# Performance work log

Measured on AMD Instinct MI355X. Metric: run time of the kernel, lower is better.

The kernel has to match this reference:

```python
import jax, jax.numpy as jnp
import numpy as np

B, H, L, N, DT_EMB, EXPAND = 8, 256, 8192, 16, 512, 2


def _tln(x, m, s):
    # TransposedLN: std/mean over channel dim (-2), population std
    mean = x.mean(axis=-2, keepdims=True)
    std = jnp.sqrt(((x - mean) ** 2).mean(axis=-2, keepdims=True))
    return s / std * (x - mean + m)


def _s4(u, log_dt, A_re, A_im, C_re, C_im, D, out_w, out_b):
    # Bidirectional diagonal S4 (S4D-style ZOH kernel) with FFT convolution.
    h, l = u.shape[-2], u.shape[-1]
    A = A_re + 1j * A_im                                   # (H, N)
    dtA = A * jnp.exp(log_dt)[:, None]                     # (H, N)
    C = (C_re + 1j * C_im) * (jnp.exp(dtA) - 1.0) / A      # (2, H, N)
    van = jnp.exp(dtA[:, :, None] * jnp.arange(l))         # (H, N, L) Vandermonde
    K = 2.0 * jnp.einsum('chn,hnl->chl', C, van).real      # (2, H, L)
    # bidirectional: forward kernel + time-flipped backward kernel, length 2L
    k = jnp.pad(K[0], ((0, 0), (0, l))) + jnp.pad(K[1][:, ::-1], ((0, 0), (l, 0)))
    y = jnp.fft.irfft(jnp.fft.rfft(u, n=2 * l) * jnp.fft.rfft(k, n=2 * l), n=2 * l)[..., :l]
    y = jax.nn.gelu(y + u * D[:, None])
    # transposed output linear (1x1 conv) H -> 2H, then GLU over channels
    z = jnp.einsum('oh,bhl->bol', out_w, y) + out_b[None, :, None]
    return z[:, :h] * jax.nn.sigmoid(z[:, h:])


def setup_inputs() -> dict:
    key = jax.random.key(0)
    ks = jax.random.split(key, 12)
    d_inner = EXPAND * H
    log_dt = jax.random.uniform(ks[0], (H,)) * (np.log(0.1) - np.log(0.001)) + np.log(0.001)
    return {
        'x': jax.random.normal(ks[1], (B, H, L), dtype=jnp.float32),
        'diffusion_step_embed': jax.random.normal(ks[2], (B, DT_EMB), dtype=jnp.float32),
        'fc_t_w': jax.random.normal(ks[3], (H, DT_EMB), dtype=jnp.float32) * 0.02,
        'fc_t_b': jnp.zeros((H,), dtype=jnp.float32),
        'log_dt': log_dt.astype(jnp.float32),
        'A_re': -0.5 * jnp.ones((H, N), dtype=jnp.float32),
        'A_im': jnp.broadcast_to(np.pi * jnp.arange(N, dtype=jnp.float32), (H, N)),
        'C_re': jax.random.normal(ks[4], (2, H, N), dtype=jnp.float32) * (0.5 ** 0.5),
        'C_im': jax.random.normal(ks[5], (2, H, N), dtype=jnp.float32) * (0.5 ** 0.5),
        'D': jax.random.normal(ks[6], (H,), dtype=jnp.float32),
        'out_w': jax.random.normal(ks[7], (2 * H, H), dtype=jnp.float32) * 0.02,
        'out_b': jnp.zeros((2 * H,), dtype=jnp.float32),
        'n1_m': jnp.zeros((), dtype=jnp.float32),
        'n1_s': jnp.ones((), dtype=jnp.float32),
        'n2_m': jnp.zeros((), dtype=jnp.float32),
        'n2_s': jnp.ones((), dtype=jnp.float32),
        'ff_w1': jax.random.normal(ks[8], (d_inner, H), dtype=jnp.float32) * 0.05,
        'ff_b1': jnp.zeros((d_inner,), dtype=jnp.float32),
        'ff_w2': jax.random.normal(ks[9], (H, d_inner), dtype=jnp.float32) * 0.05,
        'ff_b2': jnp.zeros((H,), dtype=jnp.float32),
    }


def reference(x, diffusion_step_embed, fc_t_w, fc_t_b, log_dt, A_re, A_im, C_re, C_im, D,
              out_w, out_b, n1_m, n1_s, n2_m, n2_s, ff_w1, ff_b1, ff_w2, ff_b2):
    y = _tln(x, n1_m, n1_s)
    part_t = diffusion_step_embed @ fc_t_w.T + fc_t_b      # (B, H)
    y = y + part_t[:, :, None]
    y = _s4(y, log_dt, A_re, A_im, C_re, C_im, D, out_w, out_b)
    y = x + y                                              # residual 1
    res = y
    y = _tln(y, n2_m, n2_s)
    h = jax.nn.gelu(jnp.einsum('oh,bhl->bol', ff_w1, y) + ff_b1[None, :, None])
    y = jnp.einsum('ho,bol->bhl', ff_w2, h) + ff_b2[None, :, None]
    return res + y
```

## Files before the change

kernel.cpp:

```cpp
#include <hip/hip_runtime.h>
#include <hip/hip_bf16.h>
#include <math.h>

typedef unsigned short u16;
typedef float fx4 __attribute__((ext_vector_type(4)));
typedef __bf16 bx8 __attribute__((ext_vector_type(8)));

constexpr int BB  = 8;
constexpr int HH  = 256;
constexpr int LL  = 8192;
constexpr int NN  = 16;
constexpr int DTE = 512;
constexpr int SC  = 64;
constexpr int CHN = 128;
constexpr int HN  = HH * NN;

constexpr size_t BHL = (size_t)BB * HH * LL;

constexpr int OFF_WR  = 0;
constexpr int OFF_WI  = HN;
constexpr int OFF_WSR = 2 * HN;
constexpr int OFF_WSI = 3 * HN;
constexpr int OFF_C0R = 4 * HN;
constexpr int OFF_C0I = 5 * HN;
constexpr int OFF_C1R = 6 * HN;
constexpr int OFF_C1I = 7 * HN;
constexpr int OFF_PT  = 8 * HN;

constexpr int PM_V2H = 0;
constexpr int PM_V2L = 4096;
constexpr int PM_TH  = 8192;
constexpr int PM_TL  = 12288;
constexpr int PM_CWH = 16384;
constexpr int PM_CWL = 20480;
constexpr int PM_STRIDE = 24576;

__device__ __forceinline__ float gelu_tanh(float x) {
    float x3 = x * x * x;
    float y = 1.5957691216057308f * x + 0.07135481627767453f * x3;
    return x / (1.0f + __expf(-y));
}
__device__ __forceinline__ float sigmoid_(float x) {
    return 1.0f / (1.0f + __expf(-x));
}
__device__ __forceinline__ __hip_bfloat16 f2b(float x) { return __float2bfloat16(x); }
__device__ __forceinline__ float b2f(__hip_bfloat16 x) { return __bfloat162float(x); }
__device__ __forceinline__ u16 f2us(float x) {
    __hip_bfloat16 b = __float2bfloat16(x);
    return *reinterpret_cast<u16*>(&b);
}
__device__ __forceinline__ float lo2f(unsigned v) { return __uint_as_float(v << 16); }
__device__ __forceinline__ float hi2f(unsigned v) { return __uint_as_float(v & 0xffff0000u); }
__device__ __forceinline__ unsigned pack2(float a, float b) {
    return (unsigned)f2us(a) | ((unsigned)f2us(b) << 16);
}

__global__ void setup_s4_params(const float* __restrict__ log_dt,
                                const float* __restrict__ A_re,
                                const float* __restrict__ A_im,
                                const float* __restrict__ C_re,
                                const float* __restrict__ C_im,
                                float* __restrict__ P) {
    int idx = blockIdx.x * blockDim.x + threadIdx.x;
    if (idx >= HN) return;
    int h = idx >> 4;
    double dt = exp((double)log_dt[h]);
    double Ar = (double)A_re[idx], Ai = (double)A_im[idx];
    double dr = Ar * dt, di = Ai * dt;
    double e1 = exp(dr);
    double wr = e1 * cos(di), wi = e1 * sin(di);
    double eS = exp(dr * SC);
    double wSr = eS * cos(di * SC), wSi = eS * sin(di * SC);
    double d2 = Ar * Ar + Ai * Ai;
    double nr = wr - 1.0, ni = wi;
    double rr = (nr * Ar + ni * Ai) / d2;
    double ri = (ni * Ar - nr * Ai) / d2;
    double c0r = (double)C_re[idx],        c0i = (double)C_im[idx];
    double c1r = (double)C_re[HN + idx],   c1i = (double)C_im[HN + idx];
    P[OFF_WR  + idx] = (float)wr;
    P[OFF_WI  + idx] = (float)wi;
    P[OFF_WSR + idx] = (float)wSr;
    P[OFF_WSI + idx] = (float)wSi;
    P[OFF_C0R + idx] = (float)(2.0 * (c0r * rr - c0i * ri));
    P[OFF_C0I + idx] = (float)(2.0 * (c0r * ri + c0i * rr));
    P[OFF_C1R + idx] = (float)(2.0 * (c1r * rr - c1i * ri));
    P[OFF_C1I + idx] = (float)(2.0 * (c1r * ri + c1i * rr));
}

__global__ void setup_scan_mats(const float* __restrict__ P,
                                const float* __restrict__ Dp,
                                u16* __restrict__ PM) {
    const int h = blockIdx.x;
    const int t = threadIdx.x;
    __shared__ float Wr[65][17], Wi[65][17];
    __shared__ float KF[64], KB[64];
    __shared__ float c0r[16], c0i[16], c1r[16], c1i[16];
    if (t < 16) {
        c0r[t] = P[OFF_C0R + h * NN + t]; c0i[t] = P[OFF_C0I + h * NN + t];
        c1r[t] = P[OFF_C1R + h * NN + t]; c1i[t] = P[OFF_C1I + h * NN + t];
        double wr = (double)P[OFF_WR + h * NN + t], wi = (double)P[OFF_WI + h * NN + t];
        double pr = 1.0, pi = 0.0;
        for (int tau = 0; tau <= 64; ++tau) {
            Wr[tau][t] = (float)pr; Wi[tau][t] = (float)pi;
            double nr = pr * wr - pi * wi, ni = pr * wi + pi * wr;
            pr = nr; pi = ni;
        }
    }
    __syncthreads();
    {
        float kf = 0.f, kb = 0.f;
        #pragma unroll
        for (int n = 0; n < 16; ++n) {
            kf = fmaf(c0r[n], Wr[t][n], fmaf(-c0i[n], Wi[t][n], kf));
            kb = fmaf(c1r[n], Wr[t][n], fmaf(-c1i[n], Wi[t][n], kb));
        }
        KF[t] = kf; KB[t] = kb;
    }
    __syncthreads();
    u16* base = PM + (size_t)h * PM_STRIDE;
    {
        int n = (t & 31) >> 1, reim = t & 1;
        bool fwd = t < 32;
        for (int j = 0; j < 64; ++j) {
            int e = fwd ? (63 - j) : j;
            float v = reim ? Wi[e][n] : Wr[e][n];
            __hip_bfloat16 hb = f2b(v);
            base[PM_V2H + t * 64 + j] = *(u16*)&hb;
            base[PM_V2L + t * 64 + j] = f2us(v - b2f(hb));
        }
    }
    {
        float Dh = Dp[h];
        for (int j = 0; j < 64; ++j) {
            float v = (j < t) ? KF[t - j] : ((j == t) ? (KF[0] + Dh) : KB[j - t - 1]);
            __hip_bfloat16 hb = f2b(v);
            base[PM_TH + t * 64 + j] = *(u16*)&hb;
            base[PM_TL + t * 64 + j] = f2us(v - b2f(hb));
        }
    }
    {
        #pragma unroll
        for (int n = 0; n < 16; ++n) {
            float Rw = Wr[t + 1][n], Iw = Wi[t + 1][n];
            float af = fmaf(c0r[n], Rw, -c0i[n] * Iw);
            float bf = -fmaf(c0r[n], Iw, c0i[n] * Rw);
            float Rb = Wr[63 - t][n], Ib = Wi[63 - t][n];
            float ab = fmaf(c1r[n], Rb, -c1i[n] * Ib);
            float bb = -fmaf(c1r[n], Ib, c1i[n] * Rb);
            float vals[4] = {af, bf, ab, bb};
            int cols[4] = {2 * n, 2 * n + 1, 32 + 2 * n, 32 + 2 * n + 1};
            #pragma unroll
            for (int q = 0; q < 4; ++q) {
                __hip_bfloat16 hb = f2b(vals[q]);
                base[PM_CWH + t * 64 + cols[q]] = *(u16*)&hb;
                base[PM_CWL + t * 64 + cols[q]] = f2us(vals[q] - b2f(hb));
            }
        }
    }
}

__global__ void part_t_kernel(const float* __restrict__ emb,
                              const float* __restrict__ w,
                              const float* __restrict__ bias,
                              float* __restrict__ P) {
    int idx = blockIdx.x * blockDim.x + threadIdx.x;
    if (idx >= BB * HH) return;
    int b = idx / HH, h = idx % HH;
    float s = bias[h];
    const float* er = emb + (size_t)b * DTE;
    const float* wr = w + (size_t)h * DTE;
    for (int e = 0; e < DTE; ++e) s = fmaf(er[e], wr[e], s);
    P[OFF_PT + idx] = s;
}

__global__ void convert_w_kernel(const float* __restrict__ src, u16* __restrict__ dst, int n) {
    int i = blockIdx.x * 256 + threadIdx.x;
    if (i < n) dst[i] = f2us(src[i]);
}

__global__ void convert_w_split(const float* __restrict__ src,
                                u16* __restrict__ hi, u16* __restrict__ lo, int n) {
    int i = blockIdx.x * 256 + threadIdx.x;
    if (i < n) {
        float v = src[i];
        __hip_bfloat16 hb = f2b(v);
        hi[i] = *reinterpret_cast<u16*>(&hb);
        lo[i] = f2us(v - b2f(hb));
    }
}

__global__ void tln_kernel(const float* __restrict__ in, float* __restrict__ out,
                           const float* __restrict__ mptr, const float* __restrict__ sptr,
                           const float* __restrict__ part_t) {
    int b = blockIdx.y;
    int l0 = blockIdx.x * 64;
    int t = threadIdx.x;
    int q = t >> 6, li = t & 63;
    const float* base = in + (size_t)b * HH * LL + l0 + li;
    float sum = 0.f, sq = 0.f;
    for (int i = 0; i < 64; ++i) {
        float v = base[(size_t)(q * 64 + i) * LL];
        sum += v; sq = fmaf(v, v, sq);
    }
    __shared__ float rs[4][64], rq[4][64], meanS[64], scaleS[64];
    rs[q][li] = sum; rq[q][li] = sq;
    __syncthreads();
    if (q == 0) {
        float s  = rs[0][li] + rs[1][li] + rs[2][li] + rs[3][li];
        float s2 = rq[0][li] + rq[1][li] + rq[2][li] + rq[3][li];
        float mean = s * (1.f / 256.f);
        float var  = fmaxf(s2 * (1.f / 256.f) - mean * mean, 0.f);
        meanS[li]  = mean;
        scaleS[li] = sptr[0] / sqrtf(var);
    }
    __syncthreads();
    float mean = meanS[li], scale = scaleS[li], m = mptr[0];
    float* ob = out + (size_t)b * HH * LL + l0 + li;
    for (int i = 0; i < 64; ++i) {
        int h = q * 64 + i;
        float v = base[(size_t)h * LL];
        float y = scale * (v - mean + m) + part_t[b * HH + h];
        ob[(size_t)h * LL] = y;
    }
}

__global__ void tln2t_kernel(const float* __restrict__ in, u16* __restrict__ outT,
                             const float* __restrict__ mptr, const float* __restrict__ sptr) {
    int b = blockIdx.y;
    int l0 = blockIdx.x * 64;
    int t = threadIdx.x;
    int q = t >> 6, li = t & 63;
    const float* base = in + (size_t)b * HH * LL + l0 + li;
    float sum = 0.f, sq = 0.f;
    for (int i = 0; i < 64; ++i) {
        float v = base[(size_t)(q * 64 + i) * LL];
        sum += v; sq = fmaf(v, v, sq);
    }
    __shared__ float rs[4][64], rq[4][64], meanS[64], scaleS[64];
    __shared__ u16 TT[64 * 262];
    rs[q][li] = sum; rq[q][li] = sq;
    __syncthreads();
    if (q == 0) {
        float s  = rs[0][li] + rs[1][li] + rs[2][li] + rs[3][li];
        float s2 = rq[0][li] + rq[1][li] + rq[2][li] + rq[3][li];
        float mean = s * (1.f / 256.f);
        float var  = fmaxf(s2 * (1.f / 256.f) - mean * mean, 0.f);
        meanS[li]  = mean;
        scaleS[li] = sptr[0] / sqrtf(var);
    }
    __syncthreads();
    float mean = meanS[li], scale = scaleS[li], m = mptr[0];
    for (int i = 0; i < 64; ++i) {
        int h = q * 64 + i;
        float v = base[(size_t)h * LL];
        TT[li * 262 + h] = f2us(scale * (v - mean + m));
    }
    __syncthreads();
    #pragma unroll
    for (int i = 0; i < 32; ++i) {
        int idx = t + i * 256;
        int c = idx & 127, l = idx >> 7;
        unsigned int v = *(const unsigned int*)&TT[l * 262 + 2 * c];
        *(unsigned int*)&outT[((size_t)b * LL + l0 + l) * 256 + 2 * c] = v;
    }
}

constexpr int UPAD = 136;
constexpr int SPAD = 72;

__global__ __launch_bounds__(256, 3) void scan_mfma(
    const float* __restrict__ uIn, const float* __restrict__ P,
    const u16* __restrict__ PM, float* __restrict__ ys)
{
    __shared__ __align__(16) u16 U[128 * UPAD];
    __shared__ __align__(16) u16 SES[128 * SPAD];

    const int bh  = blockIdx.x;
    const int h   = bh & (HH - 1);
    const int tid = threadIdx.x;
    const int lane = tid & 63;
    const int wq   = tid >> 6;
    const u16* pm = PM + (size_t)h * PM_STRIDE;
    const float* urow = uIn + (size_t)bh * LL;
    float* yrow = ys + (size_t)bh * LL;

    {
        const float4* u4 = (const float4*)urow;
        #pragma unroll
        for (int i = 0; i < 8; ++i) {
            int e4 = tid + i * 256;
            float4 v = u4[e4];
            int g = e4 << 2, c = g >> 6, j = g & 63;
            u16 hi4[4], lo4[4];
            #pragma unroll
            for (int q = 0; q < 4; ++q) {
                float f = (&v.x)[q];
                __hip_bfloat16 hb = f2b(f);
                hi4[q] = *(u16*)&hb;
                lo4[q] = f2us(f - b2f(hb));
            }
            *(ushort4*)&U[c * UPAD + j]      = *(ushort4*)hi4;
            *(ushort4*)&U[c * UPAD + 64 + j] = *(ushort4*)lo4;
        }
    }
    __syncthreads();

    const int cb    = wq * 32 + (lane & 15);
    const int kfrag = ((lane >> 4) & 3) * 8;
    const int arow_lo = lane & 15;

    bx8 ubh[2][2], ubl[2][2];
    #pragma unroll
    for (int nt = 0; nt < 2; ++nt) {
        int c = cb + nt * 16;
        #pragma unroll
        for (int ks = 0; ks < 2; ++ks) {
            ubh[nt][ks] = *(const bx8*)&U[c * UPAD + ks * 32 + kfrag];
            ubl[nt][ks] = *(const bx8*)&U[c * UPAD + 64 + ks * 32 + kfrag];
        }
    }

    {
        fx4 acc[4][2];
        #pragma unroll
        for (int mt = 0; mt < 4; ++mt)
            #pragma unroll
            for (int nt = 0; nt < 2; ++nt) { fx4 z = {0.f,0.f,0.f,0.f}; acc[mt][nt] = z; }
        #pragma unroll
        for (int mt = 0; mt < 4; ++mt) {
            #pragma unroll
            for (int ks = 0; ks < 2; ++ks) {
                int ao = (mt * 16 + arow_lo) * 64 + ks * 32 + kfrag;
                bx8 vh = *(const bx8*)&pm[PM_V2H + ao];
                bx8 vl = *(const bx8*)&pm[PM_V2L + ao];
                #pragma unroll
                for (int nt = 0; nt < 2; ++nt) {
                    acc[mt][nt] = __builtin_amdgcn_mfma_f32_16x16x32_bf16(vh, ubh[nt][ks], acc[mt][nt], 0, 0, 0);
                    acc[mt][nt] = __builtin_amdgcn_mfma_f32_16x16x32_bf16(vh, ubl[nt][ks], acc[mt][nt], 0, 0, 0);
                    acc[mt][nt] = __builtin_amdgcn_mfma_f32_16x16x32_bf16(vl, ubh[nt][ks], acc[mt][nt], 0, 0, 0);
                }
            }
        }
        #pragma unroll
        for (int mt = 0; mt < 4; ++mt)
            #pragma unroll
            for (int nt = 0; nt < 2; ++nt) {
                int c = cb + nt * 16;
                int row = mt * 16 + (lane >> 4) * 4;
                #pragma unroll
                for (int r = 0; r < 4; ++r)
                    SES[c * SPAD + row + r] = f2us(acc[mt][nt][r]);
            }
    }
    __syncthreads();

    if (tid < 32) {
        const int d3 = tid >> 4, n = tid & 15;
        float wSr = P[OFF_WSR + h * NN + n], wSi = P[OFF_WSI + h * NN + n];
        const int kk = d3 * 32 + 2 * n;
        float cr = 0.f, ci = 0.f;
        if (d3 == 0) {
            for (int q = 0; q < CHN; ++q) {
                unsigned* p = (unsigned*)&SES[q * SPAD + kk];
                unsigned pv = *p;
                float fr = lo2f(pv), fi = hi2f(pv);
                *p = pack2(cr, ci);
                float nr2 = fmaf(wSr, cr, fmaf(-wSi, ci, fr));
                float ni2 = fmaf(wSr, ci, fmaf(wSi, cr, fi));
                cr = nr2; ci = ni2;
            }
        } else {
            for (int q = CHN - 1; q >= 0; --q) {
                unsigned* p = (unsigned*)&SES[q * SPAD + kk];
                unsigned pv = *p;
                float fr = lo2f(pv), fi = hi2f(pv);
                *p = pack2(cr, ci);
                float nr2 = fmaf(wSr, cr, fmaf(-wSi, ci, fr));
                float ni2 = fmaf(wSr, ci, fmaf(wSi, cr, fi));
                cr = nr2; ci = ni2;
            }
        }
    }
    __syncthreads();

    {
        bx8 sb[2][2];
        #pragma unroll
        for (int nt = 0; nt < 2; ++nt) {
            int c = cb + nt * 16;
            #pragma unroll
            for (int ks = 0; ks < 2; ++ks)
                sb[nt][ks] = *(const bx8*)&SES[c * SPAD + ks * 32 + kfrag];
        }
        fx4 acc[4][2];
        #pragma unroll
        for (int mt = 0; mt < 4; ++mt)
            #pragma unroll
            for (int nt = 0; nt < 2; ++nt) { fx4 z = {0.f,0.f,0.f,0.f}; acc[mt][nt] = z; }
        #pragma unroll
        for (int mt = 0; mt < 4; ++mt) {
            #pragma unroll
            for (int ks = 0; ks < 2; ++ks) {
                int ao = (mt * 16 + arow_lo) * 64 + ks * 32 + kfrag;
                bx8 th = *(const bx8*)&pm[PM_TH + ao];
                bx8 tl = *(const bx8*)&pm[PM_TL + ao];
                bx8 ch = *(const bx8*)&pm[PM_CWH + ao];
                bx8 cl = *(const bx8*)&pm[PM_CWL + ao];
                #pragma unroll
                for (int nt = 0; nt < 2; ++nt) {
                    acc[mt][nt] = __builtin_amdgcn_mfma_f32_16x16x32_bf16(th, ubh[nt][ks], acc[mt][nt], 0, 0, 0);
                    acc[mt][nt] = __builtin_amdgcn_mfma_f32_16x16x32_bf16(th, ubl[nt][ks], acc[mt][nt], 0, 0, 0);
                    acc[mt][nt] = __builtin_amdgcn_mfma_f32_16x16x32_bf16(tl, ubh[nt][ks], acc[mt][nt], 0, 0, 0);
                    acc[mt][nt] = __builtin_amdgcn_mfma_f32_16x16x32_bf16(ch, sb[nt][ks], acc[mt][nt], 0, 0, 0);
                    acc[mt][nt] = __builtin_amdgcn_mfma_f32_16x16x32_bf16(cl, sb[nt][ks], acc[mt][nt], 0, 0, 0);
                }
            }
        }
        #pragma unroll
        for (int mt = 0; mt < 4; ++mt)
            #pragma unroll
            for (int nt = 0; nt < 2; ++nt) {
                int c = cb + nt * 16;
                float4 ov;
                #pragma unroll
                for (int r = 0; r < 4; ++r)
                    (&ov.x)[r] = gelu_tanh(acc[mt][nt][r]);
                *(float4*)&yrow[c * 64 + mt * 16 + (lane >> 4) * 4] = ov;
            }
    }
}

__global__ __launch_bounds__(256, 2) void gemm_glu_mfma(
    const u16* __restrict__ Whi, const u16* __restrict__ Wlo,
    const float* __restrict__ Y, const float* __restrict__ bias,
    const float* __restrict__ xres, float* __restrict__ out)
{
    __shared__ __align__(16) char smem[65536];
    u16* Ah = (u16*)smem;
    u16* Al = Ah + 8192;
    u16* Bh = Al + 8192;
    u16* Bl = Bh + 8192;

    const int tid  = threadIdx.x;
    const int lane = tid & 63;
    const int wv   = tid >> 6;
    const int wrh  = wv & 1;
    const int wch  = wv >> 1;
    const int bz   = blockIdx.z;
    const int l0   = blockIdx.x * 128;
    const int c0   = blockIdx.y * 64;

    fx4 acc[4][4];
    #pragma unroll
    for (int i = 0; i < 4; ++i)
        #pragma unroll
        for (int j = 0; j < 4; ++j) {
            fx4 z = {0.f, 0.f, 0.f, 0.f};
            acc[i][j] = z;
        }

    const int am  = tid & 127;
    const int akh = tid >> 7;
    const int aorow = (am < 64) ? (c0 + am) : (c0 + 256 + (am - 64));
    const int amt = am >> 4, amm = am & 15;

    const int bli = (tid & 63) + ((tid >> 6) & 1) * 64;
    const int bkh = tid >> 7;
    const int bnt = bli >> 4, bcol = bli & 15;

    const float* Yb = Y + (size_t)bz * HH * LL + l0;

    for (int k0 = 0; k0 < 256; k0 += 64) {
        #pragma unroll
        for (int oct = 0; oct < 4; ++oct) {
            int k = k0 + akh * 32 + oct * 8;
            int4 vh = *(const int4*)&Whi[(size_t)aorow * 256 + k];
            int4 vl = *(const int4*)&Wlo[(size_t)aorow * 256 + k];
            int base = ((akh * 8 + amt) * 64 + amm + (oct << 4)) * 8;
            *(int4*)&Ah[base] = vh;
            *(int4*)&Al[base] = vl;
        }
        #pragma unroll
        for (int oct = 0; oct < 4; ++oct) {
            int kb = k0 + bkh * 32 + oct * 8;
            float v[8];
            #pragma unroll
            for (int j = 0; j < 8; ++j)
                v[j] = Yb[(size_t)(kb + j) * LL + bli];
            u16 h8[8], l8[8];
            #pragma unroll
            for (int j = 0; j < 8; ++j) {
                __hip_bfloat16 hb = f2b(v[j]);
                h8[j] = *reinterpret_cast<u16*>(&hb);
                l8[j] = f2us(v[j] - b2f(hb));
            }
            int base = ((bkh * 8 + bnt) * 64 + bcol + (oct << 4)) * 8;
            *(int4*)&Bh[base] = *(const int4*)h8;
            *(int4*)&Bl[base] = *(const int4*)l8;
        }
        __syncthreads();
        #pragma unroll
        for (int ks = 0; ks < 2; ++ks) {
            bx8 bh[4], bl[4];
            #pragma unroll
            for (int nt = 0; nt < 4; ++nt) {
                int base = ((ks * 8 + wch * 4 + nt) * 64 + lane) * 8;
                bh[nt] = *(const bx8*)&Bh[base];
                bl[nt] = *(const bx8*)&Bl[base];
            }
            #pragma unroll
            for (int mt = 0; mt < 4; ++mt) {
                int base = ((ks * 8 + wrh * 4 + mt) * 64 + lane) * 8;
                bx8 ah = *(const bx8*)&Ah[base];
                bx8 al = *(const bx8*)&Al[base];
                #pragma unroll
                for (int nt = 0; nt < 4; ++nt) {
                    acc[mt][nt] = __builtin_amdgcn_mfma_f32_16x16x32_bf16(ah, bh[nt], acc[mt][nt], 0, 0, 0);
                    acc[mt][nt] = __builtin_amdgcn_mfma_f32_16x16x32_bf16(ah, bl[nt], acc[mt][nt], 0, 0, 0);
                    acc[mt][nt] = __builtin_amdgcn_mfma_f32_16x16x32_bf16(al, bh[nt], acc[mt][nt], 0, 0, 0);
                }
            }
        }
        __syncthreads();
    }

    float* zbuf = (float*)smem;
    if (wrh == 1) {
        #pragma unroll
        for (int mt = 0; mt < 4; ++mt) {
            int mloc = mt * 16 + (lane >> 4) * 4;
            float b1v[4];
            #pragma unroll
            for (int r = 0; r < 4; ++r) b1v[r] = bias[c0 + 256 + mloc + r];
            #pragma unroll
            for (int nt = 0; nt < 4; ++nt) {
                int nloc = nt * 16 + (lane & 15);
                #pragma unroll
                for (int r = 0; r < 4; ++r)
                    zbuf[wch * 4160 + (mloc + r) * 65 + nloc] = acc[mt][nt][r] + b1v[r];
            }
        }
    }
    __syncthreads();
    if (wrh == 0) {
        #pragma unroll
        for (int mt = 0; mt < 4; ++mt) {
            int mloc = mt * 16 + (lane >> 4) * 4;
            float b0v[4];
            #pragma unroll
            for (int r = 0; r < 4; ++r) b0v[r] = bias[c0 + mloc + r];
            #pragma unroll
            for (int nt = 0; nt < 4; ++nt) {
                int nloc = nt * 16 + (lane & 15);
                int l = l0 + wch * 64 + nloc;
                #pragma unroll
                for (int r = 0; r < 4; ++r) {
                    float z1 = zbuf[wch * 4160 + (mloc + r) * 65 + nloc];
                    float z0 = acc[mt][nt][r] + b0v[r];
                    size_t ga = ((size_t)bz * HH + c0 + mloc + r) * LL + l;
                    out[ga] = z0 * sigmoid_(z1) + xres[ga];
                }
            }
        }
    }
}

template<int MODE, int WLD>
__global__ __launch_bounds__(256, 3) void gemm_mfma(
    const u16* __restrict__ Aw, const u16* __restrict__ Bm,
    const float* bias, const float* resid, void* outv)
{
    __shared__ __align__(16) char smem[33792];
    u16*   Alds = (u16*)smem;
    u16*   Blds = (u16*)(smem + 16384);
    float* Eps  = (float*)smem;
    u16*   TT   = (u16*)smem;

    const int tid  = threadIdx.x;
    const int lane = tid & 63;
    const int wv   = tid >> 6;
    const int wr   = wv >> 1, wc = wv & 1;
    const int bz   = blockIdx.z;
    const int l0   = blockIdx.x * 128;
    const int mbase = blockIdx.y * 128;

    fx4 acc[4][4];
    #pragma unroll
    for (int i = 0; i < 4; ++i)
        #pragma unroll
        for (int j = 0; j < 4; ++j) {
            fx4 z = {0.f, 0.f, 0.f, 0.f};
            acc[i][j] = z;
        }

    const size_t brow0 = (size_t)bz * LL;
    for (int k0 = 0; k0 < 256; k0 += 64) {
        #pragma unroll
        for (int i = 0; i < 4; ++i) {
            int f = tid + i * 256;
            int mm = f & 15, kg = (f >> 4) & 3, m16 = (f >> 6) & 7, ks = f >> 9;
            int k = k0 + ks * 32 + kg * 8;
            int o = mbase + m16 * 16 + mm;
            int4 wv4 = *(const int4*)(Aw + (size_t)o * WLD + k);
            *(int4*)&Alds[f * 8] = wv4;
            int row = l0 + m16 * 16 + mm;
            int4 xv4 = *(const int4*)(Bm + (brow0 + row) * 256 + k);
            *(int4*)&Blds[f * 8] = xv4;
        }
        __syncthreads();
        #pragma unroll
        for (int ks = 0; ks < 2; ++ks) {
            bx8 av[4], bv[4];
            #pragma unroll
            for (int mt = 0; mt < 4; ++mt)
                av[mt] = *(const bx8*)&Alds[(ks * 512 + (wr * 4 + mt) * 64 + lane) * 8];
            #pragma unroll
            for (int nt = 0; nt < 4; ++nt)
                bv[nt] = *(const bx8*)&Blds[(ks * 512 + (wc * 4 + nt) * 64 + lane) * 8];
            #pragma unroll
            for (int mt = 0; mt < 4; ++mt)
                #pragma unroll
                for (int nt = 0; nt < 4; ++nt)
                    acc[mt][nt] = __builtin_amdgcn_mfma_f32_16x16x32_bf16(
                        av[mt], bv[nt], acc[mt][nt], 0, 0, 0);
        }
        __syncthreads();
    }

    if (MODE == 1) {
        u16* hT = (u16*)outv;
        #pragma unroll
        for (int p = 0; p < 2; ++p) {
            if (p) __syncthreads();
            if (wc == p) {
                #pragma unroll
                for (int mt = 0; mt < 4; ++mt) {
                    int mb = wr * 64 + mt * 16 + (lane >> 4) * 4;
                    float bvv[4];
                    #pragma unroll
                    for (int r = 0; r < 4; ++r) bvv[r] = bias[mbase + mb + r];
                    #pragma unroll
                    for (int nt = 0; nt < 4; ++nt) {
                        int n = nt * 16 + (lane & 15);
                        u16 pk[4];
                        #pragma unroll
                        for (int r = 0; r < 4; ++r)
                            pk[r] = f2us(gelu_tanh(acc[mt][nt][r] + bvv[r]));
                        *(ushort4*)&TT[n * 136 + mb] = *(const ushort4*)pk;
                    }
                }
            }
            __syncthreads();
            #pragma unroll
            for (int i = 0; i < 4; ++i) {
                int idx = tid + i * 256;
                int l = idx >> 4, c = idx & 15;
                int4 v = *(const int4*)&TT[l * 136 + c * 8];
                *(int4*)&hT[((size_t)bz * LL + l0 + p * 64 + l) * 256 + mbase + c * 8] = v;
            }
        }
    } else {
        float* outp = (float*)outv;
        #pragma unroll
        for (int p = 0; p < 2; ++p) {
            if (p) __syncthreads();
            if (wc == p) {
                #pragma unroll
                for (int mt = 0; mt < 4; ++mt)
                    #pragma unroll
                    for (int nt = 0; nt < 4; ++nt) {
                        int m = wr * 64 + mt * 16 + (lane >> 4) * 4;
                        int n = nt * 16 + (lane & 15);
                        #pragma unroll
                        for (int r = 0; r < 4; ++r)
                            Eps[(m + r) * 66 + n] = acc[mt][nt][r];
                    }
            }
            __syncthreads();
            #pragma unroll
            for (int i = 0; i < 8; ++i) {
                int idx = tid + i * 256;
                int r = idx >> 4, lq = idx & 15;
                float bv = bias ? bias[mbase + r] : 0.f;
                size_t ga = ((size_t)bz * HH + mbase + r) * LL + l0 + p * 64 + lq * 4;
                float4 rv = *(const float4*)&resid[ga];
                float4 ov;
                #pragma unroll
                for (int j = 0; j < 4; ++j)
                    (&ov.x)[j] = Eps[r * 66 + lq * 4 + j] + bv + (&rv.x)[j];
                *(float4*)&outp[ga] = ov;
            }
        }
    }
}

extern "C" void kernel_launch(void* const* d_in, const int* in_sizes, int n_in,
                              void* d_out, int out_size, void* d_ws, size_t ws_size,
                              hipStream_t stream) {
    (void)in_sizes; (void)n_in; (void)out_size; (void)ws_size;
    const float* x      = (const float*)d_in[0];
    const float* emb    = (const float*)d_in[1];
    const float* fc_t_w = (const float*)d_in[2];
    const float* fc_t_b = (const float*)d_in[3];
    const float* log_dt = (const float*)d_in[4];
    const float* A_re   = (const float*)d_in[5];
    const float* A_im   = (const float*)d_in[6];
    const float* C_re   = (const float*)d_in[7];
    const float* C_im   = (const float*)d_in[8];
    const float* Dp     = (const float*)d_in[9];
    const float* out_w  = (const float*)d_in[10];
    const float* out_b  = (const float*)d_in[11];
    const float* n1_m   = (const float*)d_in[12];
    const float* n1_s   = (const float*)d_in[13];
    const float* n2_m   = (const float*)d_in[14];
    const float* n2_s   = (const float*)d_in[15];
    const float* ff_w1  = (const float*)d_in[16];
    const float* ff_b1  = (const float*)d_in[17];
    const float* ff_w2  = (const float*)d_in[18];
    const float* ff_b2  = (const float*)d_in[19];
    float* outp = (float*)d_out;

    float* wsf  = (float*)d_ws;
    float* u    = wsf;
    u16*   t2T  = (u16*)wsf;
    u16*   hT   = (u16*)(wsf + BHL);
    u16*   PM   = (u16*)(wsf + BHL + BHL / 2);
    constexpr size_t WPOFF = 2 * BHL - 524288;
    u16*   W1c  = (u16*)(wsf + WPOFF);
    u16*   W2c  = W1c + 131072;
    u16*   WOh  = W2c + 131072;
    u16*   WOl  = WOh + 131072;
    float* P    = wsf + WPOFF + 262144;

    setup_s4_params<<<16, 256, 0, stream>>>(log_dt, A_re, A_im, C_re, C_im, P);
    part_t_kernel<<<8, 256, 0, stream>>>(emb, fc_t_w, fc_t_b, P);
    setup_scan_mats<<<HH, 64, 0, stream>>>(P, Dp, PM);
    convert_w_kernel<<<512, 256, 0, stream>>>(ff_w1, W1c, 512 * 256);
    convert_w_kernel<<<512, 256, 0, stream>>>(ff_w2, W2c, 256 * 512);
    convert_w_split<<<512, 256, 0, stream>>>(out_w, WOh, WOl, 512 * 256);

    tln_kernel<<<dim3(LL / 64, BB), 256, 0, stream>>>(x, u, n1_m, n1_s, P + OFF_PT);

    scan_mfma<<<BB * HH, 256, 0, stream>>>(u, P, PM, u);

    gemm_glu_mfma<<<dim3(LL / 128, 4, BB), 256, 0, stream>>>(WOh, WOl, u, out_b, x, outp);

    tln2t_kernel<<<dim3(LL / 64, BB), 256, 0, stream>>>(outp, t2T, n2_m, n2_s);

    gemm_mfma<1, 256><<<dim3(LL / 128, 2, BB), 256, 0, stream>>>(W1c, t2T, ff_b1, nullptr, hT);
    gemm_mfma<2, 512><<<dim3(LL / 128, 2, BB), 256, 0, stream>>>(W2c, hT, ff_b2, outp, outp);
    gemm_mfma<1, 256><<<dim3(LL / 128, 2, BB), 256, 0, stream>>>(W1c + 65536, t2T, ff_b1 + 256, nullptr, hT);
    gemm_mfma<2, 512><<<dim3(LL / 128, 2, BB), 256, 0, stream>>>(W2c + 256, hT, nullptr, outp, outp);
}
```

Measured before the change: 537.4 us.

## Register-prefetch next K tile in GEMM kernels and shrink GLU LDS tile

Both MFMA GEMM kernels now load the next K-slice from global memory into registers right after the barrier, so the loads overlap with the current slice's MFMA work. The GLU GEMM also halves its K tile from 64 to 32, which cuts shared memory to about 33 KB and raises the occupancy hint to 3 blocks per CU. The trade-offs are twice as many barriers per tile in the GLU kernel, plus extra register pressure from the prefetch buffers that could cause spills under the tighter launch bound.

```diff
diff --git a/kernel.cpp b/kernel.cpp
--- a/kernel.cpp
+++ b/kernel.cpp
@@ -430,16 +430,16 @@
     }
 }
 
-__global__ __launch_bounds__(256, 2) void gemm_glu_mfma(
+__global__ __launch_bounds__(256, 3) void gemm_glu_mfma(
     const u16* __restrict__ Whi, const u16* __restrict__ Wlo,
     const float* __restrict__ Y, const float* __restrict__ bias,
     const float* __restrict__ xres, float* __restrict__ out)
 {
-    __shared__ __align__(16) char smem[65536];
+    __shared__ __align__(16) char smem[33792];
     u16* Ah = (u16*)smem;
-    u16* Al = Ah + 8192;
-    u16* Bh = Al + 8192;
-    u16* Bl = Bh + 8192;
+    u16* Al = Ah + 4096;
+    u16* Bh = Al + 4096;
+    u16* Bl = Bh + 4096;
 
     const int tid  = threadIdx.x;
     const int lane = tid & 63;
@@ -459,64 +459,91 @@
             acc[i][j] = z;
         }
 
-    const int am  = tid & 127;
-    const int akh = tid >> 7;
+    const int am   = tid & 127;
+    const int aob  = (tid >> 7) * 2;
     const int aorow = (am < 64) ? (c0 + am) : (c0 + 256 + (am - 64));
-    const int amt = am >> 4, amm = am & 15;
-
-    const int bli = (tid & 63) + ((tid >> 6) & 1) * 64;
-    const int bkh = tid >> 7;
-    const int bnt = bli >> 4, bcol = bli & 15;
-
-    const float* Yb = Y + (size_t)bz * HH * LL + l0;
-
-    for (int k0 = 0; k0 < 256; k0 += 64) {
-        #pragma unroll
-        for (int oct = 0; oct < 4; ++oct) {
-            int k = k0 + akh * 32 + oct * 8;
-            int4 vh = *(const int4*)&Whi[(size_t)aorow * 256 + k];
-            int4 vl = *(const int4*)&Wlo[(size_t)aorow * 256 + k];
-            int base = ((akh * 8 + amt) * 64 + amm + (oct << 4)) * 8;
-            *(int4*)&Ah[base] = vh;
-            *(int4*)&Al[base] = vl;
-        }
-        #pragma unroll
-        for (int oct = 0; oct < 4; ++oct) {
-            int kb = k0 + bkh * 32 + oct * 8;
-            float v[8];
-            #pragma unroll
-            for (int j = 0; j < 8; ++j)
-                v[j] = Yb[(size_t)(kb + j) * LL + bli];
+    const int aldsbase = (am >> 4) * 64 + (am & 15);
+
+    const int blc  = tid & 127;
+    const int bob  = (tid >> 7) * 2;
+    const int bldsbase = (blc >> 4) * 64 + (blc & 15);
+
+    const float* Yb = Y + (size_t)bz * HH * LL + l0 + blc;
+
+    int4 rAh[2], rAl[2];
+    float rB[16];
+
+    #pragma unroll 1
+    for (int kt = 0; kt < 8; ++kt) {
+        if (kt == 0) {
+            #pragma unroll
+            for (int o = 0; o < 2; ++o) {
+                int k = (aob + o) * 8;
+                rAh[o] = *(const int4*)&Whi[(size_t)aorow * 256 + k];
+                rAl[o] = *(const int4*)&Wlo[(size_t)aorow * 256 + k];
+            }
+            #pragma unroll
+            for (int o = 0; o < 2; ++o) {
+                int kb = (bob + o) * 8;
+                #pragma unroll
+                for (int j = 0; j < 8; ++j)
+                    rB[o * 8 + j] = Yb[(size_t)(kb + j) * LL];
+            }
+        }
+        #pragma unroll
+        for (int o = 0; o < 2; ++o) {
+            int idx = (aldsbase + (aob + o) * 16) * 8;
+            *(int4*)&Ah[idx] = rAh[o];
+            *(int4*)&Al[idx] = rAl[o];
+        }
+        #pragma unroll
+        for (int o = 0; o < 2; ++o) {
             u16 h8[8], l8[8];
             #pragma unroll
             for (int j = 0; j < 8; ++j) {
-                __hip_bfloat16 hb = f2b(v[j]);
-                h8[j] = *reinterpret_cast<u16*>(&hb);
-                l8[j] = f2us(v[j] - b2f(hb));
-            }
-            int base = ((bkh * 8 + bnt) * 64 + bcol + (oct << 4)) * 8;
-            *(int4*)&Bh[base] = *(const int4*)h8;
-            *(int4*)&Bl[base] = *(const int4*)l8;
+                float v = rB[o * 8 + j];
+                __hip_bfloat16 hb = f2b(v);
+                h8[j] = *(u16*)&hb;
+                l8[j] = f2us(v - b2f(hb));
+            }
+            int idx = (bldsbase + (bob + o) * 16) * 8;
+            *(int4*)&Bh[idx] = *(const int4*)h8;
+            *(int4*)&Bl[idx] = *(const int4*)l8;
         }
         __syncthreads();
-        #pragma unroll
-        for (int ks = 0; ks < 2; ++ks) {
-            bx8 bh[4], bl[4];
+        if (kt < 7) {
+            int k0 = (kt + 1) * 32;
+            #pragma unroll
+            for (int o = 0; o < 2; ++o) {
+                int k = k0 + (aob + o) * 8;
+                rAh[o] = *(const int4*)&Whi[(size_t)aorow * 256 + k];
+                rAl[o] = *(const int4*)&Wlo[(size_t)aorow * 256 + k];
+            }
+            #pragma unroll
+            for (int o = 0; o < 2; ++o) {
+                int kb = k0 + (bob + o) * 8;
+                #pragma unroll
+                for (int j = 0; j < 8; ++j)
+                    rB[o * 8 + j] = Yb[(size_t)(kb + j) * LL];
+            }
+        }
+        {
+            bx8 bh[4], blv[4];
             #pragma unroll
             for (int nt = 0; nt < 4; ++nt) {
-                int base = ((ks * 8 + wch * 4 + nt) * 64 + lane) * 8;
-                bh[nt] = *(const bx8*)&Bh[base];
-                bl[nt] = *(const bx8*)&Bl[base];
+                int base = ((wch * 4 + nt) * 64 + lane) * 8;
+                bh[nt]  = *(const bx8*)&Bh[base];
+                blv[nt] = *(const bx8*)&Bl[base];
             }
             #pragma unroll
             for (int mt = 0; mt < 4; ++mt) {
-                int base = ((ks * 8 + wrh * 4 + mt) * 64 + lane) * 8;
+                int base = ((wrh * 4 + mt) * 64 + lane) * 8;
                 bx8 ah = *(const bx8*)&Ah[base];
                 bx8 al = *(const bx8*)&Al[base];
                 #pragma unroll
                 for (int nt = 0; nt < 4; ++nt) {
                     acc[mt][nt] = __builtin_amdgcn_mfma_f32_16x16x32_bf16(ah, bh[nt], acc[mt][nt], 0, 0, 0);
-                    acc[mt][nt] = __builtin_amdgcn_mfma_f32_16x16x32_bf16(ah, bl[nt], acc[mt][nt], 0, 0, 0);
+                    acc[mt][nt] = __builtin_amdgcn_mfma_f32_16x16x32_bf16(ah, blv[nt], acc[mt][nt], 0, 0, 0);
                     acc[mt][nt] = __builtin_amdgcn_mfma_f32_16x16x32_bf16(al, bh[nt], acc[mt][nt], 0, 0, 0);
                 }
             }
@@ -594,20 +621,38 @@
         }
 
     const size_t brow0 = (size_t)bz * LL;
-    for (int k0 = 0; k0 < 256; k0 += 64) {
+    int4 rA[4], rB[4];
+
+    #pragma unroll 1
+    for (int kt = 0; kt < 4; ++kt) {
+        if (kt == 0) {
+            #pragma unroll
+            for (int i = 0; i < 4; ++i) {
+                int f = tid + i * 256;
+                int mm = f & 15, kg = (f >> 4) & 3, m16 = (f >> 6) & 7, ks = f >> 9;
+                int k = ks * 32 + kg * 8;
+                rA[i] = *(const int4*)(Aw + (size_t)(mbase + m16 * 16 + mm) * WLD + k);
+                rB[i] = *(const int4*)(Bm + (brow0 + l0 + m16 * 16 + mm) * 256 + k);
+            }
+        }
         #pragma unroll
         for (int i = 0; i < 4; ++i) {
             int f = tid + i * 256;
-            int mm = f & 15, kg = (f >> 4) & 3, m16 = (f >> 6) & 7, ks = f >> 9;
-            int k = k0 + ks * 32 + kg * 8;
-            int o = mbase + m16 * 16 + mm;
-            int4 wv4 = *(const int4*)(Aw + (size_t)o * WLD + k);
-            *(int4*)&Alds[f * 8] = wv4;
-            int row = l0 + m16 * 16 + mm;
-            int4 xv4 = *(const int4*)(Bm + (brow0 + row) * 256 + k);
-            *(int4*)&Blds[f * 8] = xv4;
+            *(int4*)&Alds[f * 8] = rA[i];
+            *(int4*)&Blds[f * 8] = rB[i];
         }
         __syncthreads();
+        if (kt < 3) {
+            int k0 = (kt + 1) * 64;
+            #pragma unroll
+            for (int i = 0; i < 4; ++i) {
+                int f = tid + i * 256;
+                int mm = f & 15, kg = (f >> 4) & 3, m16 = (f >> 6) & 7, ks = f >> 9;
+                int k = k0 + ks * 32 + kg * 8;
+                rA[i] = *(const int4*)(Aw + (size_t)(mbase + m16 * 16 + mm) * WLD + k);
+                rB[i] = *(const int4*)(Bm + (brow0 + l0 + m16 * 16 + mm) * 256 + k);
+            }
+        }
         #pragma unroll
         for (int ks = 0; ks < 2; ++ks) {
             bx8 av[4], bv[4];
```

New measurement: 770.3 us. +43.3%, slower.

## Fuse feed-forward GEMM pair into one kernel keeping hidden activations in LDS

Applied to the files above, without the earlier changes.

Replaces the four separate FF GEMM launches, which round-trip the bf16 hidden tensor through global memory, with one fused kernel. Each block loads a 64-column input tile into LDS, computes hidden chunks with GELU into LDS, and accumulates the second GEMM in registers. Weights are pre-swizzled into MFMA fragment order so the kernel can read them directly from global memory without LDS staging. The cost is that weights are re-read per block, and the epilogue writes are less coalesced scalar stores.

```diff
diff --git a/kernel.cpp b/kernel.cpp
--- a/kernel.cpp
+++ b/kernel.cpp
@@ -173,11 +173,6 @@
     P[OFF_PT + idx] = s;
 }
 
-__global__ void convert_w_kernel(const float* __restrict__ src, u16* __restrict__ dst, int n) {
-    int i = blockIdx.x * 256 + threadIdx.x;
-    if (i < n) dst[i] = f2us(src[i]);
-}
-
 __global__ void convert_w_split(const float* __restrict__ src,
                                 u16* __restrict__ hi, u16* __restrict__ lo, int n) {
     int i = blockIdx.x * 256 + threadIdx.x;
@@ -187,6 +182,20 @@
         hi[i] = *reinterpret_cast<u16*>(&hb);
         lo[i] = f2us(v - b2f(hb));
     }
+}
+
+__global__ void convert_w_frag(const float* __restrict__ src, u16* __restrict__ dst,
+                               int KS, int Ktot) {
+    int b = blockIdx.x;
+    int lane = threadIdx.x;
+    int mi = b / KS, ks = b % KS;
+    int row = mi * 16 + (lane & 15);
+    int col = ks * 32 + (lane >> 4) * 8;
+    const float* s = src + (size_t)row * Ktot + col;
+    u16 pk[8];
+    #pragma unroll
+    for (int j = 0; j < 8; ++j) pk[j] = f2us(s[j]);
+    *(int4*)&dst[((size_t)b * 64 + lane) * 8] = *(const int4*)pk;
 }
 
 __global__ void tln_kernel(const float* __restrict__ in, float* __restrict__ out,
@@ -565,130 +574,120 @@
     }
 }
 
-template<int MODE, int WLD>
-__global__ __launch_bounds__(256, 3) void gemm_mfma(
-    const u16* __restrict__ Aw, const u16* __restrict__ Bm,
-    const float* bias, const float* resid, void* outv)
+__global__ __launch_bounds__(256, 3) void ff_fused(
+    const u16* __restrict__ W1f, const u16* __restrict__ W2f,
+    const u16* __restrict__ Xt,
+    const float* __restrict__ b1, const float* __restrict__ b2,
+    float* __restrict__ io)
 {
-    __shared__ __align__(16) char smem[33792];
-    u16*   Alds = (u16*)smem;
-    u16*   Blds = (u16*)(smem + 16384);
-    float* Eps  = (float*)smem;
-    u16*   TT   = (u16*)smem;
+    __shared__ __align__(16) u16 Xf[64 * 256];
+    __shared__ __align__(16) u16 Hf[8192];
 
     const int tid  = threadIdx.x;
     const int lane = tid & 63;
-    const int wv   = tid >> 6;
-    const int wr   = wv >> 1, wc = wv & 1;
-    const int bz   = blockIdx.z;
-    const int l0   = blockIdx.x * 128;
-    const int mbase = blockIdx.y * 128;
-
-    fx4 acc[4][4];
+    const int w    = tid >> 6;
+    const int lq   = lane >> 4;
+    const int l15  = lane & 15;
+    const int bz   = blockIdx.y;
+    const int l0   = blockIdx.x * 64;
+
+    {
+        const int li = tid >> 2;
+        const int cq = (tid & 3) * 64;
+        const u16* srcp = Xt + ((size_t)bz * LL + l0 + li) * 256 + cq;
+        const int nt = li >> 4, ll = li & 15;
+        #pragma unroll
+        for (int i = 0; i < 8; ++i) {
+            int c = cq + i * 8;
+            int4 v = *(const int4*)(srcp + i * 8);
+            int addr = ((nt * 8 + (c >> 5)) * 64 + ((c >> 3) & 3) * 16 + ll) * 8;
+            *(int4*)&Xf[addr] = v;
+        }
+    }
+    __syncthreads();
+
+    fx4 acc2[4][4];
     #pragma unroll
     for (int i = 0; i < 4; ++i)
         #pragma unroll
         for (int j = 0; j < 4; ++j) {
             fx4 z = {0.f, 0.f, 0.f, 0.f};
-            acc[i][j] = z;
-        }
-
-    const size_t brow0 = (size_t)bz * LL;
-    for (int k0 = 0; k0 < 256; k0 += 64) {
-        #pragma unroll
-        for (int i = 0; i < 4; ++i) {
-            int f = tid + i * 256;
-            int mm = f & 15, kg = (f >> 4) & 3, m16 = (f >> 6) & 7, ks = f >> 9;
-            int k = k0 + ks * 32 + kg * 8;
-            int o = mbase + m16 * 16 + mm;
-            int4 wv4 = *(const int4*)(Aw + (size_t)o * WLD + k);
-            *(int4*)&Alds[f * 8] = wv4;
-            int row = l0 + m16 * 16 + mm;
-            int4 xv4 = *(const int4*)(Bm + (brow0 + row) * 256 + k);
-            *(int4*)&Blds[f * 8] = xv4;
+            acc2[i][j] = z;
+        }
+
+    #pragma unroll 1
+    for (int hc = 0; hc < 4; ++hc) {
+        fx4 acc1[2][4];
+        #pragma unroll
+        for (int i = 0; i < 2; ++i)
+            #pragma unroll
+            for (int j = 0; j < 4; ++j) {
+                fx4 z = {0.f, 0.f, 0.f, 0.f};
+                acc1[i][j] = z;
+            }
+        #pragma unroll
+        for (int ks = 0; ks < 8; ++ks) {
+            bx8 xb[4];
+            #pragma unroll
+            for (int nt = 0; nt < 4; ++nt)
+                xb[nt] = *(const bx8*)&Xf[((nt * 8 + ks) * 64 + lane) * 8];
+            #pragma unroll
+            for (int mt = 0; mt < 2; ++mt) {
+                int mi = hc * 8 + w * 2 + mt;
+                bx8 a = *(const bx8*)&W1f[((size_t)(mi * 8 + ks) * 64 + lane) * 8];
+                #pragma unroll
+                for (int nt = 0; nt < 4; ++nt)
+                    acc1[mt][nt] = __builtin_amdgcn_mfma_f32_16x16x32_bf16(a, xb[nt], acc1[mt][nt], 0, 0, 0);
+            }
         }
         __syncthreads();
         #pragma unroll
-        for (int ks = 0; ks < 2; ++ks) {
-            bx8 av[4], bv[4];
-            #pragma unroll
-            for (int mt = 0; mt < 4; ++mt)
-                av[mt] = *(const bx8*)&Alds[(ks * 512 + (wr * 4 + mt) * 64 + lane) * 8];
+        for (int mt = 0; mt < 2; ++mt) {
+            int hbase = hc * 128 + w * 32 + mt * 16 + lq * 4;
+            float bb[4];
+            #pragma unroll
+            for (int r = 0; r < 4; ++r) bb[r] = b1[hbase + r];
+            #pragma unroll
+            for (int nt = 0; nt < 4; ++nt) {
+                u16 pk[4];
+                #pragma unroll
+                for (int r = 0; r < 4; ++r)
+                    pk[r] = f2us(gelu_tanh(acc1[mt][nt][r] + bb[r]));
+                int addr = ((nt * 4 + w) * 64 + (mt * 2 + (lq >> 1)) * 16 + l15) * 8 + (lq & 1) * 4;
+                *(ushort4*)&Hf[addr] = *(const ushort4*)pk;
+            }
+        }
+        __syncthreads();
+        #pragma unroll
+        for (int ks = 0; ks < 4; ++ks) {
+            bx8 hb[4];
             #pragma unroll
             for (int nt = 0; nt < 4; ++nt)
-                bv[nt] = *(const bx8*)&Blds[(ks * 512 + (wc * 4 + nt) * 64 + lane) * 8];
-            #pragma unroll
-            for (int mt = 0; mt < 4; ++mt)
+                hb[nt] = *(const bx8*)&Hf[((nt * 4 + ks) * 64 + lane) * 8];
+            #pragma unroll
+            for (int mt2 = 0; mt2 < 4; ++mt2) {
+                int mi2 = w * 4 + mt2, kk = hc * 4 + ks;
+                bx8 a = *(const bx8*)&W2f[((size_t)(mi2 * 16 + kk) * 64 + lane) * 8];
                 #pragma unroll
                 for (int nt = 0; nt < 4; ++nt)
-                    acc[mt][nt] = __builtin_amdgcn_mfma_f32_16x16x32_bf16(
-                        av[mt], bv[nt], acc[mt][nt], 0, 0, 0);
-        }
-        __syncthreads();
-    }
-
-    if (MODE == 1) {
-        u16* hT = (u16*)outv;
-        #pragma unroll
-        for (int p = 0; p < 2; ++p) {
-            if (p) __syncthreads();
-            if (wc == p) {
-                #pragma unroll
-                for (int mt = 0; mt < 4; ++mt) {
-                    int mb = wr * 64 + mt * 16 + (lane >> 4) * 4;
-                    float bvv[4];
-                    #pragma unroll
-                    for (int r = 0; r < 4; ++r) bvv[r] = bias[mbase + mb + r];
-                    #pragma unroll
-                    for (int nt = 0; nt < 4; ++nt) {
-                        int n = nt * 16 + (lane & 15);
-                        u16 pk[4];
-                        #pragma unroll
-                        for (int r = 0; r < 4; ++r)
-                            pk[r] = f2us(gelu_tanh(acc[mt][nt][r] + bvv[r]));
-                        *(ushort4*)&TT[n * 136 + mb] = *(const ushort4*)pk;
-                    }
-                }
-            }
-            __syncthreads();
-            #pragma unroll
-            for (int i = 0; i < 4; ++i) {
-                int idx = tid + i * 256;
-                int l = idx >> 4, c = idx & 15;
-                int4 v = *(const int4*)&TT[l * 136 + c * 8];
-                *(int4*)&hT[((size_t)bz * LL + l0 + p * 64 + l) * 256 + mbase + c * 8] = v;
-            }
-        }
-    } else {
-        float* outp = (float*)outv;
-        #pragma unroll
-        for (int p = 0; p < 2; ++p) {
-            if (p) __syncthreads();
-            if (wc == p) {
-                #pragma unroll
-                for (int mt = 0; mt < 4; ++mt)
-                    #pragma unroll
-                    for (int nt = 0; nt < 4; ++nt) {
-                        int m = wr * 64 + mt * 16 + (lane >> 4) * 4;
-                        int n = nt * 16 + (lane & 15);
-                        #pragma unroll
-                        for (int r = 0; r < 4; ++r)
-                            Eps[(m + r) * 66 + n] = acc[mt][nt][r];
-                    }
-            }
-            __syncthreads();
-            #pragma unroll
-            for (int i = 0; i < 8; ++i) {
-                int idx = tid + i * 256;
-                int r = idx >> 4, lq = idx & 15;
-                float bv = bias ? bias[mbase + r] : 0.f;
-                size_t ga = ((size_t)bz * HH + mbase + r) * LL + l0 + p * 64 + lq * 4;
-                float4 rv = *(const float4*)&resid[ga];
-                float4 ov;
-                #pragma unroll
-                for (int j = 0; j < 4; ++j)
-                    (&ov.x)[j] = Eps[r * 66 + lq * 4 + j] + bv + (&rv.x)[j];
-                *(float4*)&outp[ga] = ov;
+                    acc2[mt2][nt] = __builtin_amdgcn_mfma_f32_16x16x32_bf16(a, hb[nt], acc2[mt2][nt], 0, 0, 0);
+            }
+        }
+    }
+
+    #pragma unroll
+    for (int mt2 = 0; mt2 < 4; ++mt2) {
+        int m = w * 64 + mt2 * 16 + lq * 4;
+        float b2v[4];
+        #pragma unroll
+        for (int r = 0; r < 4; ++r) b2v[r] = b2[m + r];
+        #pragma unroll
+        for (int nt = 0; nt < 4; ++nt) {
+            int n = l0 + nt * 16 + l15;
+            #pragma unroll
+            for (int r = 0; r < 4; ++r) {
+                size_t ga = ((size_t)bz * HH + m + r) * LL + n;
+                io[ga] = acc2[mt2][nt][r] + b2v[r] + io[ga];
             }
         }
     }
@@ -723,20 +722,19 @@
     float* wsf  = (float*)d_ws;
     float* u    = wsf;
     u16*   t2T  = (u16*)wsf;
-    u16*   hT   = (u16*)(wsf + BHL);
     u16*   PM   = (u16*)(wsf + BHL + BHL / 2);
     constexpr size_t WPOFF = 2 * BHL - 524288;
-    u16*   W1c  = (u16*)(wsf + WPOFF);
-    u16*   W2c  = W1c + 131072;
-    u16*   WOh  = W2c + 131072;
+    u16*   W1f  = (u16*)(wsf + WPOFF);
+    u16*   W2f  = W1f + 131072;
+    u16*   WOh  = W2f + 131072;
     u16*   WOl  = WOh + 131072;
     float* P    = wsf + WPOFF + 262144;
 
     setup_s4_params<<<16, 256, 0, stream>>>(log_dt, A_re, A_im, C_re, C_im, P);
     part_t_kernel<<<8, 256, 0, stream>>>(emb, fc_t_w, fc_t_b, P);
     setup_scan_mats<<<HH, 64, 0, stream>>>(P, Dp, PM);
-    convert_w_kernel<<<512, 256, 0, stream>>>(ff_w1, W1c, 512 * 256);
-    convert_w_kernel<<<512, 256, 0, stream>>>(ff_w2, W2c, 256 * 512);
+    convert_w_frag<<<256, 64, 0, stream>>>(ff_w1, W1f, 8, 256);
+    convert_w_frag<<<256, 64, 0, stream>>>(ff_w2, W2f, 16, 512);
     convert_w_split<<<512, 256, 0, stream>>>(out_w, WOh, WOl, 512 * 256);
 
     tln_kernel<<<dim3(LL / 64, BB), 256, 0, stream>>>(x, u, n1_m, n1_s, P + OFF_PT);
@@ -747,8 +745,5 @@
 
     tln2t_kernel<<<dim3(LL / 64, BB), 256, 0, stream>>>(outp, t2T, n2_m, n2_s);
 
-    gemm_mfma<1, 256><<<dim3(LL / 128, 2, BB), 256, 0, stream>>>(W1c, t2T, ff_b1, nullptr, hT);
-    gemm_mfma<2, 512><<<dim3(LL / 128, 2, BB), 256, 0, stream>>>(W2c, hT, ff_b2, outp, outp);
-    gemm_mfma<1, 256><<<dim3(LL / 128, 2, BB), 256, 0, stream>>>(W1c + 65536, t2T, ff_b1 + 256, nullptr, hT);
-    gemm_mfma<2, 512><<<dim3(LL / 128, 2, BB), 256, 0, stream>>>(W2c + 256, hT, nullptr, outp, outp);
-}
+    ff_fused<<<dim3(LL / 64, BB), 256, 0, stream>>>(W1f, W2f, t2T, ff_b1, ff_b2, outp);
+}
```

After: 513.8 us. 1.05x faster.
